# Kernel tuning notes

Hardware: AMD Instinct MI355X
Metric: run time of the kernel (lower is better)

## Reference

```python
import jax, jax.numpy as jnp
import numpy as np

B, T, D, H = 4, 2048, 1024, 16
HD = D // H  # head_size = 64
EPS = 1e-5


def layernorm(x, g, b):
    mu = jnp.mean(x, axis=-1, keepdims=True)
    var = jnp.var(x, axis=-1, keepdims=True)
    return (x - mu) * jax.lax.rsqrt(var + EPS) * g + b


def setup_inputs() -> dict:
    key = jax.random.key(0)
    ks = jax.random.split(key, 8)
    s = 0.02
    return {
        "x": jax.random.normal(ks[0], (B, T, D), jnp.float32),
        "Wq": jax.random.normal(ks[1], (D, D), jnp.float32) * s,
        "Wk": jax.random.normal(ks[2], (D, D), jnp.float32) * s,
        "Wv": jax.random.normal(ks[3], (D, D), jnp.float32) * s,
        "Wo": jax.random.normal(ks[4], (D, D), jnp.float32) * s,
        "bo": jnp.zeros((D,), jnp.float32),
        "W1": jax.random.normal(ks[5], (D, 4 * D), jnp.float32) * s,
        "b1": jnp.zeros((4 * D,), jnp.float32),
        "W2": jax.random.normal(ks[6], (4 * D, D), jnp.float32) * s,
        "b2": jnp.zeros((D,), jnp.float32),
        "ln1_g": jnp.ones((D,), jnp.float32),
        "ln1_b": jnp.zeros((D,), jnp.float32),
        "ln2_g": jnp.ones((D,), jnp.float32),
        "ln2_b": jnp.zeros((D,), jnp.float32),
    }


def reference(x, Wq, Wk, Wv, Wo, bo, W1, b1, W2, b2, ln1_g, ln1_b, ln2_g, ln2_b):
    # --- multi-head causal self-attention (pre-LN), dropout off (eval) ---
    h = layernorm(x, ln1_g, ln1_b)
    q = jnp.einsum('btd,de->bte', h, Wq).reshape(B, T, H, HD)
    k = jnp.einsum('btd,de->bte', h, Wk).reshape(B, T, H, HD)
    v = jnp.einsum('btd,de->bte', h, Wv).reshape(B, T, H, HD)
    scores = jnp.einsum('bqhd,bkhd->bhqk', q, k) * (HD ** -0.5)
    causal = jnp.tril(jnp.ones((T, T), bool))
    scores = jnp.where(causal, scores, -jnp.inf)
    attn = jax.nn.softmax(scores, axis=-1)
    out = jnp.einsum('bhqk,bkhd->bqhd', attn, v).reshape(B, T, D)
    out = jnp.einsum('btd,de->bte', out, Wo) + bo
    x = x + out
    # --- feed-forward: Linear -> ReLU -> Linear -> ReLU (as in source) ---
    h2 = layernorm(x, ln2_g, ln2_b)
    ff = jax.nn.relu(jnp.einsum('btd,df->btf', h2, W1) + b1)
    ff = jax.nn.relu(jnp.einsum('btf,fd->btd', ff, W2) + b2)
    return x + ff
```

## Files before the change

### kernel.cpp

```cpp
#include <hip/hip_runtime.h>
#include <cstdint>
#include <cstddef>

typedef unsigned short u16;
typedef __attribute__((ext_vector_type(8))) short bf16x8;
typedef __attribute__((ext_vector_type(4))) float f32x4;
typedef __attribute__((address_space(1))) const unsigned int gu32;
typedef __attribute__((address_space(3))) unsigned int lu32;

#define QSCALE 0.1803368801111204f

__device__ __forceinline__ u16 f2bf(float f) {
  uint32_t u = __float_as_uint(f);
  u += 0x7fffu + ((u >> 16) & 1u);
  return (u16)(u >> 16);
}

__global__ __launch_bounds__(256) void transpose_w(const float* __restrict__ W,
                                                   u16* __restrict__ WT,
                                                   int K, int N) {
  __shared__ float t[32][33];
  int n0 = blockIdx.x * 32, k0 = blockIdx.y * 32;
  for (int i = threadIdx.y; i < 32; i += 8)
    t[i][threadIdx.x] = W[(size_t)(k0 + i) * N + n0 + threadIdx.x];
  __syncthreads();
  for (int i = threadIdx.y; i < 32; i += 8)
    WT[(size_t)(n0 + i) * K + k0 + threadIdx.x] = f2bf(t[threadIdx.x][i]);
}

__global__ __launch_bounds__(256) void ln_kernel(const float* __restrict__ x,
                                                 const float* __restrict__ g,
                                                 const float* __restrict__ b,
                                                 u16* __restrict__ out) {
  int row = blockIdx.x;
  const float4 v = *(const float4*)(x + (size_t)row * 1024 + threadIdx.x * 4);
  float s = v.x + v.y + v.z + v.w;
  float ss = v.x * v.x + v.y * v.y + v.z * v.z + v.w * v.w;
#pragma unroll
  for (int d = 1; d < 64; d <<= 1) { s += __shfl_xor(s, d); ss += __shfl_xor(ss, d); }
  __shared__ float rs_[4], rss_[4];
  int wv = threadIdx.x >> 6;
  if ((threadIdx.x & 63) == 0) { rs_[wv] = s; rss_[wv] = ss; }
  __syncthreads();
  s = rs_[0] + rs_[1] + rs_[2] + rs_[3];
  ss = rss_[0] + rss_[1] + rss_[2] + rss_[3];
  float mu = s * (1.f / 1024.f);
  float var = ss * (1.f / 1024.f) - mu * mu;
  float rstd = rsqrtf(var + 1e-5f);
  float4 gv = *(const float4*)(g + threadIdx.x * 4);
  float4 bv = *(const float4*)(b + threadIdx.x * 4);
  uint32_t lo = (uint32_t)f2bf((v.x - mu) * rstd * gv.x + bv.x) |
                ((uint32_t)f2bf((v.y - mu) * rstd * gv.y + bv.y) << 16);
  uint32_t hi = (uint32_t)f2bf((v.z - mu) * rstd * gv.z + bv.z) |
                ((uint32_t)f2bf((v.w - mu) * rstd * gv.w + bv.w) << 16);
  uint2 o; o.x = lo; o.y = hi;
  *(uint2*)(out + (size_t)row * 1024 + threadIdx.x * 4) = o;
}

#define STAGEA(slot, tnext, is)                                               \
  __builtin_amdgcn_global_load_lds(                                           \
      (gu32*)((const char*)(A + (size_t)(bm * 256 + (is) * 64 + srow) * K +   \
                            (size_t)(tnext) * 64) + ssw),                     \
      (lu32*)&lds[(slot) * 24576 + (is) * 4096 + wid * 512], 16, 0, 0)
#define STAGEB(slot, tnext, is)                                               \
  __builtin_amdgcn_global_load_lds(                                           \
      (gu32*)((const char*)(BT + (size_t)(bn * 128 + (is) * 64 + srow) * K +  \
                            (size_t)(tnext) * 64) + ssw),                     \
      (lu32*)&lds[(slot) * 24576 + 16384 + (is) * 4096 + wid * 512], 16, 0, 0)

template <int MODE>
__global__ __launch_bounds__(512, 2) void gemm8p(
    const u16* __restrict__ A, const u16* __restrict__ BT,
    int M, int N, int K,
    const float* __restrict__ bias, const float* __restrict__ resid,
    float* __restrict__ outf,
    u16* __restrict__ ob0, u16* __restrict__ ob1, u16* __restrict__ ob2) {
  __shared__ __align__(16) u16 lds[73728];
  const int tid = threadIdx.x, lane = tid & 63, wid = tid >> 6;
  const int wr = wid >> 1, wc = wid & 1;
  const int bm = blockIdx.y, bn = blockIdx.x;
  const int l15 = lane & 15, lhi = lane >> 4;
  const int srow = tid >> 3;
  const int ssw = ((tid & 7) * 16) ^ ((srow & 7) << 4);
  const int cs0 = (lhi * 8) ^ ((l15 & 7) << 3);
  const int cs1 = (32 + lhi * 8) ^ ((l15 & 7) << 3);
  const int arow = (wr * 64 + l15) * 64;
  const int brow = (wc * 64 + l15) * 64;

  f32x4 acc[4][4];
#pragma unroll
  for (int i = 0; i < 4; ++i)
#pragma unroll
    for (int j = 0; j < 4; ++j) acc[i][j] = (f32x4){0.f, 0.f, 0.f, 0.f};

  const int NT = K >> 6;

#pragma unroll
  for (int t0 = 0; t0 < 2; ++t0) {
    STAGEA(t0, t0, 0); STAGEA(t0, t0, 1); STAGEA(t0, t0, 2); STAGEA(t0, t0, 3);
    STAGEB(t0, t0, 0); STAGEB(t0, t0, 1);
  }
  asm volatile("s_waitcnt vmcnt(6)" ::: "memory");
  __builtin_amdgcn_s_barrier();

  int s = 0, sn = 2;
  for (int t = 0; t < NT; ++t) {
    const bool hasPre = (t + 2) < NT;
    const int aoff = s * 24576, boff = s * 24576 + 16384;

    bf16x8 bfr[4][2], afr[2][2];
#pragma unroll
    for (int ni = 0; ni < 4; ++ni) {
      bfr[ni][0] = *(const bf16x8*)&lds[boff + brow + ni * 1024 + cs0];
      bfr[ni][1] = *(const bf16x8*)&lds[boff + brow + ni * 1024 + cs1];
    }
    afr[0][0] = *(const bf16x8*)&lds[aoff + arow + cs0];
    afr[0][1] = *(const bf16x8*)&lds[aoff + arow + cs1];
    afr[1][0] = *(const bf16x8*)&lds[aoff + arow + 1024 + cs0];
    afr[1][1] = *(const bf16x8*)&lds[aoff + arow + 1024 + cs1];
    if (hasPre) { STAGEA(sn, t + 2, 0); STAGEA(sn, t + 2, 1); STAGEB(sn, t + 2, 0); }
    __builtin_amdgcn_s_barrier();
    __builtin_amdgcn_s_setprio(1);
#pragma unroll
    for (int ks = 0; ks < 2; ++ks)
#pragma unroll
      for (int ml = 0; ml < 2; ++ml)
#pragma unroll
        for (int ni = 0; ni < 4; ++ni)
          acc[ml][ni] = __builtin_amdgcn_mfma_f32_16x16x32_bf16(afr[ml][ks], bfr[ni][ks], acc[ml][ni], 0, 0, 0);
    __builtin_amdgcn_s_setprio(0);
    __builtin_amdgcn_s_barrier();

    afr[0][0] = *(const bf16x8*)&lds[aoff + arow + 2048 + cs0];
    afr[0][1] = *(const bf16x8*)&lds[aoff + arow + 2048 + cs1];
    afr[1][0] = *(const bf16x8*)&lds[aoff + arow + 3072 + cs0];
    afr[1][1] = *(const bf16x8*)&lds[aoff + arow + 3072 + cs1];
    if (hasPre) { STAGEA(sn, t + 2, 2); STAGEA(sn, t + 2, 3); STAGEB(sn, t + 2, 1); }
    __builtin_amdgcn_s_barrier();
    __builtin_amdgcn_s_setprio(1);
#pragma unroll
    for (int ks = 0; ks < 2; ++ks)
#pragma unroll
      for (int ml = 0; ml < 2; ++ml)
#pragma unroll
        for (int ni = 0; ni < 4; ++ni)
          acc[2 + ml][ni] = __builtin_amdgcn_mfma_f32_16x16x32_bf16(afr[ml][ks], bfr[ni][ks], acc[2 + ml][ni], 0, 0, 0);
    __builtin_amdgcn_s_setprio(0);
    if (hasPre) {
      asm volatile("s_waitcnt vmcnt(6)" ::: "memory");
    } else if (t + 1 < NT) {
      asm volatile("s_waitcnt vmcnt(0)" ::: "memory");
    }
    __builtin_amdgcn_s_barrier();

    s = (s == 2) ? 0 : s + 1;
    sn = (sn == 2) ? 0 : sn + 1;
  }

  if (MODE == 0) {
    char* ep = (char*)lds;
    const bool vmode = (bn >= 16);
    if (vmode) {
#pragma unroll
      for (int mi = 0; mi < 4; ++mi)
#pragma unroll
        for (int ni = 0; ni < 4; ++ni) {
          uint32_t lo, hi;
          asm("v_cvt_pk_bf16_f32 %0, %1, %2"
              : "=v"(lo) : "v"(acc[mi][ni][0]), "v"(acc[mi][ni][1]));
          asm("v_cvt_pk_bf16_f32 %0, %1, %2"
              : "=v"(hi) : "v"(acc[mi][ni][2]), "v"(acc[mi][ni][3]));
          uint2 pk; pk.x = lo; pk.y = hi;
          int c_local = wc * 64 + ni * 16 + l15;
          int rb = wr * 64 + mi * 16 + lhi * 4;
          *(uint2*)(ep + c_local * 528 + rb * 2) = pk;
        }
    } else {
      const float sc = (bn < 8) ? QSCALE : 1.f;
#pragma unroll
      for (int mi = 0; mi < 4; ++mi)
#pragma unroll
        for (int ni = 0; ni < 4; ++ni) {
          int c_local = wc * 64 + ni * 16 + l15;
          int rb = wr * 64 + mi * 16 + lhi * 4;
#pragma unroll
          for (int r = 0; r < 4; ++r) {
            *(u16*)(ep + (rb + r) * 272 + c_local * 2) = f2bf(acc[mi][ni][r] * sc);
          }
        }
    }
    __syncthreads();
    if (vmode) {
#pragma unroll
      for (int i = 0; i < 8; ++i) {
        int idx = i * 512 + tid;
        int c = idx >> 5, tc = idx & 31;
        uint4 d4 = *(const uint4*)(ep + c * 528 + tc * 16);
        int cm = bn * 128 + c - 2048, hh = cm >> 6, dd = cm & 63;
        size_t bh = (size_t)((bm >> 3) * 16 + hh);
        int t0 = (bm & 7) * 256;
        *(uint4*)&ob2[(bh * 64 + dd) * 2048 + t0 + tc * 8] = d4;
      }
    } else {
#pragma unroll
      for (int i = 0; i < 8; ++i) {
        int idx = i * 512 + tid;
        int row = idx >> 4, cc = idx & 15;
        uint4 d4 = *(const uint4*)(ep + row * 272 + cc * 16);
        size_t rg = (size_t)(bm * 256 + row);
        int colg = bn * 128 + cc * 8;
        if (colg < 1024)
          *(uint4*)&ob0[rg * 1024 + colg] = d4;
        else
          *(uint4*)&ob1[rg * 1024 + colg - 1024] = d4;
      }
    }
  } else {
#pragma unroll
    for (int mi = 0; mi < 4; ++mi) {
#pragma unroll
      for (int ni = 0; ni < 4; ++ni) {
        int col = bn * 128 + wc * 64 + ni * 16 + l15;
        int rbase = bm * 256 + wr * 64 + mi * 16 + lhi * 4;
#pragma unroll
        for (int r = 0; r < 4; ++r) {
          float v = acc[mi][ni][r];
          int rg = rbase + r;
          if (MODE == 1) {
            outf[(size_t)rg * N + col] = v + bias[col] + resid[(size_t)rg * N + col];
          } else {
            outf[(size_t)rg * N + col] = fmaxf(v + bias[col], 0.f) + resid[(size_t)rg * N + col];
          }
        }
      }
    }
  }
}

#define SA256(buf, t, is)                                                     \
  __builtin_amdgcn_global_load_lds(                                           \
      (gu32*)((const char*)(A + (size_t)(bm * 256 + (is) * 64 + srow) * K +   \
                            (size_t)(t) * 64) + ssw),                         \
      (lu32*)&lds[(buf) * 32768 + (is) * 4096 + wid * 512], 16, 0, 0)
#define SB256(buf, t, is)                                                     \
  __builtin_amdgcn_global_load_lds(                                           \
      (gu32*)((const char*)(BT + (size_t)(bn * 256 + (is) * 64 + srow) * K +  \
                            (size_t)(t) * 64) + ssw),                         \
      (lu32*)&lds[(buf) * 32768 + 16384 + (is) * 4096 + wid * 512], 16, 0, 0)

__global__ __launch_bounds__(512, 2) void gemm256(
    const u16* __restrict__ A, const u16* __restrict__ BT,
    int M, int N, int K,
    const float* __restrict__ bias, u16* __restrict__ out) {
  __shared__ __align__(16) u16 lds[65536];
  const int tid = threadIdx.x, lane = tid & 63, wid = tid >> 6;
  const int wr = wid >> 2, wc = wid & 3;
  const int bm = blockIdx.y, bn = blockIdx.x;
  const int l15 = lane & 15, lhi = lane >> 4;
  const int srow = tid >> 3;
  const int ssw = ((tid & 7) * 16) ^ ((srow & 7) << 4);
  const int rsw = (l15 & 7) << 4;
  const int cbyte0 = (lhi * 16) ^ rsw;
  const int cbyte1 = (64 + lhi * 16) ^ rsw;

  f32x4 acc[8][4];
#pragma unroll
  for (int i = 0; i < 8; ++i)
#pragma unroll
    for (int j = 0; j < 4; ++j) acc[i][j] = (f32x4){0.f, 0.f, 0.f, 0.f};

  const int NT = K >> 6;

#pragma unroll
  for (int is = 0; is < 4; ++is) SA256(0, 0, is);
#pragma unroll
  for (int is = 0; is < 4; ++is) SB256(0, 0, is);
  asm volatile("s_waitcnt vmcnt(0)" ::: "memory");
  __builtin_amdgcn_s_barrier();

  for (int t = 0; t < NT; ++t) {
    const int buf = t & 1;
    const char* Ap = (const char*)lds + buf * 65536;
    const char* Bp = Ap + 32768;
    const bool hasNext = (t + 1) < NT;

    bf16x8 bfr[4], afr[4];
#pragma unroll
    for (int ph = 0; ph < 4; ++ph) {
      const int ks = ph >> 1, mg = ph & 1;
      const int cb = ks ? cbyte1 : cbyte0;
      if (mg == 0) {
#pragma unroll
        for (int ni = 0; ni < 4; ++ni)
          bfr[ni] = *(const bf16x8*)(Bp + (wc * 64 + ni * 16 + l15) * 128 + cb);
      }
#pragma unroll
      for (int i = 0; i < 4; ++i)
        afr[i] = *(const bf16x8*)(Ap + (wr * 128 + (mg * 4 + i) * 16 + l15) * 128 + cb);
      if (ph == 0 && hasNext) {
        SA256(buf ^ 1, t + 1, 0); SA256(buf ^ 1, t + 1, 1);
        SA256(buf ^ 1, t + 1, 2); SA256(buf ^ 1, t + 1, 3);
        SB256(buf ^ 1, t + 1, 0); SB256(buf ^ 1, t + 1, 1);
        SB256(buf ^ 1, t + 1, 2); SB256(buf ^ 1, t + 1, 3);
      }
      __builtin_amdgcn_s_barrier();
      __builtin_amdgcn_s_setprio(1);
#pragma unroll
      for (int i = 0; i < 4; ++i)
#pragma unroll
        for (int ni = 0; ni < 4; ++ni)
          acc[mg * 4 + i][ni] = __builtin_amdgcn_mfma_f32_16x16x32_bf16(afr[i], bfr[ni], acc[mg * 4 + i][ni], 0, 0, 0);
      __builtin_amdgcn_s_setprio(0);
      if (ph == 3 && hasNext) asm volatile("s_waitcnt vmcnt(0)" ::: "memory");
      __builtin_amdgcn_s_barrier();
    }
  }

  char* ep = (char*)lds;
#pragma unroll
  for (int h = 0; h < 2; ++h) {
    __syncthreads();
    if (wr == h) {
#pragma unroll
      for (int ni = 0; ni < 4; ++ni) {
        int c_local = wc * 64 + ni * 16 + l15;
        float bv = bias[bn * 256 + c_local];
#pragma unroll
        for (int mi = 0; mi < 8; ++mi) {
          int rb = mi * 16 + lhi * 4;
#pragma unroll
          for (int r = 0; r < 4; ++r) {
            float v = fmaxf(acc[mi][ni][r] + bv, 0.f);
            *(u16*)(ep + (rb + r) * 528 + c_local * 2) = f2bf(v);
          }
        }
      }
    }
    __syncthreads();
#pragma unroll
    for (int i = 0; i < 8; ++i) {
      int idx = i * 512 + tid;
      int row = idx >> 5, cc = idx & 31;
      uint4 d4 = *(const uint4*)(ep + row * 528 + cc * 16);
      size_t rg = (size_t)(bm * 256 + h * 128 + row);
      *(uint4*)&out[rg * (size_t)N + bn * 256 + cc * 8] = d4;
    }
  }
}

__global__ __launch_bounds__(512) void attn_kernel(
    const u16* __restrict__ Qb, const u16* __restrict__ Kb,
    const u16* __restrict__ VTb, u16* __restrict__ O) {
  const int p = blockIdx.x;
  const int bh = blockIdx.y;
  const int b = bh >> 4, h = bh & 15;
  const u16* Q = Qb + (size_t)b * 2048 * 1024 + h * 64;
  const u16* Kn = Kb + (size_t)b * 2048 * 1024 + h * 64;
  const u16* VT = VTb + (size_t)bh * 64 * 2048;
  const int tid = threadIdx.x, lane = tid & 63, wv = tid >> 6;
  const int l15 = lane & 15, lhi = lane >> 4;
  const int srow = tid >> 3;
  const int scol16 = (tid & 7) * 16;
  const int sw = scol16 ^ ((srow & 7) << 4);
  const int rswz = (l15 & 7) << 4;
  const int cb0 = (lhi * 16) ^ rswz;
  const int cb1 = (64 + lhi * 16) ^ rswz;

  __shared__ __align__(16) u16 KV[2][2][4096];
  __shared__ u16 Ps[8][16 * 72];

#define STAGEKV(slot, kt)                                                     \
  do {                                                                        \
    __builtin_amdgcn_global_load_lds(                                         \
        (gu32*)((const char*)(Kn + (size_t)((kt)*64 + srow) * 1024) + sw),    \
        (lu32*)&KV[slot][0][wv * 512], 16, 0, 0);                             \
    __builtin_amdgcn_global_load_lds(                                         \
        (gu32*)((const char*)(VT + (size_t)srow * 2048 + (kt)*64) + sw),      \
        (lu32*)&KV[slot][1][wv * 512], 16, 0, 0);                             \
  } while (0)

#pragma unroll
  for (int pass = 0; pass < 2; ++pass) {
    const int chunk = pass ? p : (15 - p);
    const int qbase = chunk * 128 + wv * 16;
    const int nkt = 2 * chunk + 2;

    bf16x8 qf[2];
#pragma unroll
    for (int ks = 0; ks < 2; ++ks)
      qf[ks] = *(const bf16x8*)&Q[(size_t)(qbase + l15) * 1024 + ks * 32 + lhi * 8];

    f32x4 o[4];
#pragma unroll
    for (int f = 0; f < 4; ++f) o[f] = (f32x4){0.f, 0.f, 0.f, 0.f};
    float m = -1e30f;
    float l = 0.f;

    __syncthreads();
    STAGEKV(0, 0);

    for (int kt = 0; kt < nkt; ++kt) {
      const int cs = kt & 1;
      asm volatile("s_waitcnt vmcnt(0)" ::: "memory");
      __syncthreads();
      if (kt + 1 < nkt) STAGEKV(cs ^ 1, kt + 1);

      if (kt * 64 <= qbase + 15) {
        const char* Kbase = (const char*)&KV[cs][0][0];
        const char* Vbase = (const char*)&KV[cs][1][0];

        f32x4 s[4];
#pragma unroll
        for (int jt = 0; jt < 4; ++jt) s[jt] = (f32x4){0.f, 0.f, 0.f, 0.f};
        __builtin_amdgcn_s_setprio(1);
#pragma unroll
        for (int ks = 0; ks < 2; ++ks) {
          const int cbyte = ks ? cb1 : cb0;
#pragma unroll
          for (int jt = 0; jt < 4; ++jt) {
            bf16x8 kf = *(const bf16x8*)(Kbase + (jt * 16 + l15) * 128 + cbyte);
            s[jt] = __builtin_amdgcn_mfma_f32_16x16x32_bf16(kf, qf[ks], s[jt], 0, 0, 0);
          }
        }
        __builtin_amdgcn_s_setprio(0);

        if (kt * 64 + 63 > qbase) {
          int qg = qbase + l15;
#pragma unroll
          for (int jt = 0; jt < 4; ++jt)
#pragma unroll
            for (int r = 0; r < 4; ++r) {
              int kg = kt * 64 + jt * 16 + lhi * 4 + r;
              if (kg > qg) s[jt][r] = -1e30f;
            }
        }

        float mr = fmaxf(fmaxf(s[0][0], s[0][1]), fmaxf(s[0][2], s[0][3]));
#pragma unroll
        for (int jt = 1; jt < 4; ++jt)
          mr = fmaxf(mr, fmaxf(fmaxf(s[jt][0], s[jt][1]), fmaxf(s[jt][2], s[jt][3])));
        mr = fmaxf(mr, __shfl_xor(mr, 16));
        mr = fmaxf(mr, __shfl_xor(mr, 32));
        if (__any(mr > m + 8.f)) {
          float mn = fmaxf(m, mr);
          float sc = exp2f(m - mn);
          l *= sc;
          m = mn;
#pragma unroll
          for (int r = 0; r < 4; ++r) {
            float so = __shfl(sc, lhi * 4 + r);
#pragma unroll
            for (int f = 0; f < 4; ++f) o[f][r] *= so;
          }
        }

        float rs = 0.f;
#pragma unroll
        for (int jt = 0; jt < 4; ++jt)
#pragma unroll
          for (int r = 0; r < 4; ++r) {
            float pv = exp2f(s[jt][r] - m);
            s[jt][r] = pv;
            rs += pv;
          }
        rs += __shfl_xor(rs, 16);
        rs += __shfl_xor(rs, 32);
        l += rs;

#pragma unroll
        for (int jt = 0; jt < 4; ++jt) {
          uint32_t lo, hi;
          asm("v_cvt_pk_bf16_f32 %0, %1, %2"
              : "=v"(lo) : "v"(s[jt][0]), "v"(s[jt][1]));
          asm("v_cvt_pk_bf16_f32 %0, %1, %2"
              : "=v"(hi) : "v"(s[jt][2]), "v"(s[jt][3]));
          uint2 pk; pk.x = lo; pk.y = hi;
          *(uint2*)&Ps[wv][l15 * 72 + jt * 16 + lhi * 4] = pk;
        }
        __builtin_amdgcn_s_setprio(1);
#pragma unroll
        for (int ks = 0; ks < 2; ++ks) {
          const int cbyte = ks ? cb1 : cb0;
          bf16x8 pf = *(const bf16x8*)&Ps[wv][l15 * 72 + ks * 32 + lhi * 8];
#pragma unroll
          for (int f = 0; f < 4; ++f) {
            bf16x8 vfr = *(const bf16x8*)(Vbase + (f * 16 + l15) * 128 + cbyte);
            o[f] = __builtin_amdgcn_mfma_f32_16x16x32_bf16(pf, vfr, o[f], 0, 0, 0);
          }
        }
        __builtin_amdgcn_s_setprio(0);
      }
    }

#pragma unroll
    for (int r = 0; r < 4; ++r) {
      float ld = __shfl(l, lhi * 4 + r);
      float inv = 1.f / ld;
      int t = qbase + lhi * 4 + r;
#pragma unroll
      for (int f = 0; f < 4; ++f)
        O[((size_t)(b * 2048 + t)) * 1024 + h * 64 + f * 16 + l15] = f2bf(o[f][r] * inv);
    }
  }
#undef STAGEKV
}

extern "C" void kernel_launch(void* const* d_in, const int* in_sizes, int n_in,
                              void* d_out, int out_size, void* d_ws, size_t ws_size,
                              hipStream_t stream) {
  const float* x   = (const float*)d_in[0];
  const float* Wq  = (const float*)d_in[1];
  const float* Wk  = (const float*)d_in[2];
  const float* Wv  = (const float*)d_in[3];
  const float* Wo  = (const float*)d_in[4];
  const float* bo  = (const float*)d_in[5];
  const float* W1  = (const float*)d_in[6];
  const float* b1  = (const float*)d_in[7];
  const float* W2  = (const float*)d_in[8];
  const float* b2  = (const float*)d_in[9];
  const float* g1  = (const float*)d_in[10];
  const float* be1 = (const float*)d_in[11];
  const float* g2  = (const float*)d_in[12];
  const float* be2 = (const float*)d_in[13];

  char* p = (char*)d_ws;
  auto alloc = [&](size_t bytes) {
    char* r = p;
    p += (bytes + 255) & ~(size_t)255;
    return r;
  };
  u16* WqkvT = (u16*)alloc(3072ull * 1024 * 2);
  u16* WoT   = (u16*)alloc(1024ull * 1024 * 2);
  u16* W1T   = (u16*)alloc(4096ull * 1024 * 2);
  u16* W2T   = (u16*)alloc(1024ull * 4096 * 2);
  u16* hln   = (u16*)alloc(8192ull * 1024 * 2);
  u16* Qbuf  = (u16*)alloc(8192ull * 1024 * 2);
  u16* Kbuf  = (u16*)alloc(8192ull * 1024 * 2);
  u16* VTbuf = (u16*)alloc(8192ull * 1024 * 2);
  float* x2  = (float*)alloc(8192ull * 1024 * 4);
  u16* ff1   = (u16*)alloc(8192ull * 4096 * 2);
  u16* Oattn = hln;
  u16* h2    = Qbuf;
  if ((size_t)(p - (char*)d_ws) > ws_size) return;

  dim3 tb(32, 8);
  transpose_w<<<dim3(32, 32), tb, 0, stream>>>(Wq, WqkvT, 1024, 1024);
  transpose_w<<<dim3(32, 32), tb, 0, stream>>>(Wk, WqkvT + 1024 * 1024, 1024, 1024);
  transpose_w<<<dim3(32, 32), tb, 0, stream>>>(Wv, WqkvT + 2048 * 1024, 1024, 1024);
  transpose_w<<<dim3(32, 32), tb, 0, stream>>>(Wo, WoT, 1024, 1024);
  transpose_w<<<dim3(128, 32), tb, 0, stream>>>(W1, W1T, 1024, 4096);
  transpose_w<<<dim3(32, 128), tb, 0, stream>>>(W2, W2T, 4096, 1024);

  ln_kernel<<<8192, 256, 0, stream>>>(x, g1, be1, hln);

  gemm8p<0><<<dim3(24, 32), 512, 0, stream>>>(hln, WqkvT, 8192, 3072, 1024,
                                              nullptr, nullptr, nullptr,
                                              Qbuf, Kbuf, VTbuf);

  attn_kernel<<<dim3(8, 64), 512, 0, stream>>>(Qbuf, Kbuf, VTbuf, Oattn);

  gemm8p<1><<<dim3(8, 32), 512, 0, stream>>>(Oattn, WoT, 8192, 1024, 1024,
                                             bo, x, x2, nullptr, nullptr, nullptr);

  ln_kernel<<<8192, 256, 0, stream>>>(x2, g2, be2, h2);

  gemm256<<<dim3(16, 32), 512, 0, stream>>>(h2, W1T, 8192, 4096, 1024, b1, ff1);

  gemm8p<3><<<dim3(8, 32), 512, 0, stream>>>(ff1, W2T, 8192, 1024, 4096,
                                             b2, x2, (float*)d_out, nullptr, nullptr, nullptr);
}
```

Measured before the change: 393.0 us.

## Rework FFN1 GEMM into a 4-slot K=32 pipeline with three loads in flight

The 256x256 FFN1 GEMM now uses 32-wide K tiles and four LDS slots with a three-stage prefetch instead of a 64-wide K tile with double buffering. Graded vmcnt waits replace the full drain, and each step needs one barrier pair. The aim is to keep more global-to-LDS loads in flight and hide memory latency better. In exchange there are twice as many loop iterations, each doing less MFMA work per barrier, and a new swizzle pattern that could cause LDS bank conflicts.

```diff
diff --git a/kernel.cpp b/kernel.cpp
--- a/kernel.cpp
+++ b/kernel.cpp
@@ -237,18 +237,20 @@
   }
 }
 
-#define SA256(buf, t, is)                                                     \
+#define SA32(slot, t, inst)                                                   \
   __builtin_amdgcn_global_load_lds(                                           \
-      (gu32*)((const char*)(A + (size_t)(bm * 256 + (is) * 64 + srow) * K +   \
-                            (size_t)(t) * 64) + ssw),                         \
-      (lu32*)&lds[(buf) * 32768 + (is) * 4096 + wid * 512], 16, 0, 0)
-#define SB256(buf, t, is)                                                     \
+      (gu32*)((const char*)(A + (size_t)(bm * 256 + (inst) * 128 +            \
+                            (tid >> 2)) * K + (size_t)(t) * 32) + ssw2),      \
+      (lu32*)&lds[(slot) * 16384 + (inst) * 4096 + tid * 8], 16, 0, 0)
+#define SB32(slot, t, inst)                                                   \
   __builtin_amdgcn_global_load_lds(                                           \
-      (gu32*)((const char*)(BT + (size_t)(bn * 256 + (is) * 64 + srow) * K +  \
-                            (size_t)(t) * 64) + ssw),                         \
-      (lu32*)&lds[(buf) * 32768 + 16384 + (is) * 4096 + wid * 512], 16, 0, 0)
-
-__global__ __launch_bounds__(512, 2) void gemm256(
+      (gu32*)((const char*)(BT + (size_t)(bn * 256 + (inst) * 128 +           \
+                            (tid >> 2)) * K + (size_t)(t) * 32) + ssw2),      \
+      (lu32*)&lds[(slot) * 16384 + 8192 + (inst) * 4096 + tid * 8], 16, 0, 0)
+#define STAGE32(slot, t)                                                      \
+  do { SA32(slot, t, 0); SA32(slot, t, 1); SB32(slot, t, 0); SB32(slot, t, 1); } while (0)
+
+__global__ __launch_bounds__(512, 2) void gemm256k32(
     const u16* __restrict__ A, const u16* __restrict__ BT,
     int M, int N, int K,
     const float* __restrict__ bias, u16* __restrict__ out) {
@@ -257,11 +259,8 @@
   const int wr = wid >> 2, wc = wid & 3;
   const int bm = blockIdx.y, bn = blockIdx.x;
   const int l15 = lane & 15, lhi = lane >> 4;
-  const int srow = tid >> 3;
-  const int ssw = ((tid & 7) * 16) ^ ((srow & 7) << 4);
-  const int rsw = (l15 & 7) << 4;
-  const int cbyte0 = (lhi * 16) ^ rsw;
-  const int cbyte1 = (64 + lhi * 16) ^ rsw;
+  const int ssw2 = ((tid & 3) * 16) ^ (((tid >> 2) & 3) << 4);
+  const int cb = (lhi * 16) ^ ((l15 & 3) << 4);
 
   f32x4 acc[8][4];
 #pragma unroll
@@ -269,51 +268,36 @@
 #pragma unroll
     for (int j = 0; j < 4; ++j) acc[i][j] = (f32x4){0.f, 0.f, 0.f, 0.f};
 
-  const int NT = K >> 6;
-
-#pragma unroll
-  for (int is = 0; is < 4; ++is) SA256(0, 0, is);
-#pragma unroll
-  for (int is = 0; is < 4; ++is) SB256(0, 0, is);
-  asm volatile("s_waitcnt vmcnt(0)" ::: "memory");
-  __builtin_amdgcn_s_barrier();
+  const int NT = K >> 5;
+
+  STAGE32(0, 0); STAGE32(1, 1); STAGE32(2, 2);
 
   for (int t = 0; t < NT; ++t) {
-    const int buf = t & 1;
-    const char* Ap = (const char*)lds + buf * 65536;
-    const char* Bp = Ap + 32768;
-    const bool hasNext = (t + 1) < NT;
-
-    bf16x8 bfr[4], afr[4];
-#pragma unroll
-    for (int ph = 0; ph < 4; ++ph) {
-      const int ks = ph >> 1, mg = ph & 1;
-      const int cb = ks ? cbyte1 : cbyte0;
-      if (mg == 0) {
-#pragma unroll
-        for (int ni = 0; ni < 4; ++ni)
-          bfr[ni] = *(const bf16x8*)(Bp + (wc * 64 + ni * 16 + l15) * 128 + cb);
-      }
-#pragma unroll
-      for (int i = 0; i < 4; ++i)
-        afr[i] = *(const bf16x8*)(Ap + (wr * 128 + (mg * 4 + i) * 16 + l15) * 128 + cb);
-      if (ph == 0 && hasNext) {
-        SA256(buf ^ 1, t + 1, 0); SA256(buf ^ 1, t + 1, 1);
-        SA256(buf ^ 1, t + 1, 2); SA256(buf ^ 1, t + 1, 3);
-        SB256(buf ^ 1, t + 1, 0); SB256(buf ^ 1, t + 1, 1);
-        SB256(buf ^ 1, t + 1, 2); SB256(buf ^ 1, t + 1, 3);
-      }
-      __builtin_amdgcn_s_barrier();
-      __builtin_amdgcn_s_setprio(1);
-#pragma unroll
-      for (int i = 0; i < 4; ++i)
-#pragma unroll
-        for (int ni = 0; ni < 4; ++ni)
-          acc[mg * 4 + i][ni] = __builtin_amdgcn_mfma_f32_16x16x32_bf16(afr[i], bfr[ni], acc[mg * 4 + i][ni], 0, 0, 0);
-      __builtin_amdgcn_s_setprio(0);
-      if (ph == 3 && hasNext) asm volatile("s_waitcnt vmcnt(0)" ::: "memory");
-      __builtin_amdgcn_s_barrier();
-    }
+    if (t + 3 < NT) STAGE32((t + 3) & 3, t + 3);
+    const int ahead = NT - 1 - t;
+    if (ahead >= 3)      asm volatile("s_waitcnt vmcnt(12)" ::: "memory");
+    else if (ahead == 2) asm volatile("s_waitcnt vmcnt(8)" ::: "memory");
+    else if (ahead == 1) asm volatile("s_waitcnt vmcnt(4)" ::: "memory");
+    else                 asm volatile("s_waitcnt vmcnt(0)" ::: "memory");
+    __builtin_amdgcn_s_barrier();
+
+    const char* Ap = (const char*)lds + (size_t)(t & 3) * 32768;
+    const char* Bp = Ap + 16384;
+    bf16x8 bfr[4], afr[8];
+#pragma unroll
+    for (int nf = 0; nf < 4; ++nf)
+      bfr[nf] = *(const bf16x8*)(Bp + (wc * 64 + nf * 16 + l15) * 64 + cb);
+#pragma unroll
+    for (int mf = 0; mf < 8; ++mf)
+      afr[mf] = *(const bf16x8*)(Ap + (wr * 128 + mf * 16 + l15) * 64 + cb);
+    __builtin_amdgcn_s_setprio(1);
+#pragma unroll
+    for (int mf = 0; mf < 8; ++mf)
+#pragma unroll
+      for (int nf = 0; nf < 4; ++nf)
+        acc[mf][nf] = __builtin_amdgcn_mfma_f32_16x16x32_bf16(afr[mf], bfr[nf], acc[mf][nf], 0, 0, 0);
+    __builtin_amdgcn_s_setprio(0);
+    __builtin_amdgcn_s_barrier();
   }
 
   char* ep = (char*)lds;
@@ -564,7 +548,7 @@
 
   ln_kernel<<<8192, 256, 0, stream>>>(x2, g2, be2, h2);
 
-  gemm256<<<dim3(16, 32), 512, 0, stream>>>(h2, W1T, 8192, 4096, 1024, b1, ff1);
+  gemm256k32<<<dim3(16, 32), 512, 0, stream>>>(h2, W1T, 8192, 4096, 1024, b1, ff1);
 
   gemm8p<3><<<dim3(8, 32), 512, 0, stream>>>(ff1, W2T, 8192, 1024, 4096,
                                              b2, x2, (float*)d_out, nullptr, nullptr, nullptr);
```

After: 400.8 us. No clear change (+2.0%).
